# Optimization experiments

Hardware: AMD Instinct MI355X
Metric: run time of the kernel (lower is better)

The kernel has to match this reference:

```python
import jax, jax.numpy as jnp
import numpy as np

B, N, C_IN, C_OUT = 4, 2048, 1024, 1024


def setup_inputs() -> dict:
    key = jax.random.key(0)
    ks = jax.random.split(key, 4)
    scale = 1.0 / np.sqrt(C_IN)
    return {
        "hidden_states": jax.random.normal(ks[0], (B, N, C_IN), dtype=jnp.float32),
        "Wq": jax.random.normal(ks[1], (C_OUT, C_IN), dtype=jnp.float32) * scale,
        "bq": jnp.zeros((C_OUT,), dtype=jnp.float32),
        "Wk": jax.random.normal(ks[2], (C_OUT, C_IN), dtype=jnp.float32) * scale,
        "bk": jnp.zeros((C_OUT,), dtype=jnp.float32),
        "Wv": jax.random.normal(ks[3], (C_OUT, C_IN), dtype=jnp.float32) * scale,
        "bv": jnp.zeros((C_OUT,), dtype=jnp.float32),
    }


def reference(hidden_states, Wq, bq, Wk, bk, Wv, bv):
    # torch nn.Linear: y = x @ W.T + b
    Q = jnp.einsum("bnc,dc->bnd", hidden_states, Wq) + bq
    K = jnp.einsum("bnc,dc->bnd", hidden_states, Wk) + bk
    V = jnp.einsum("bnc,dc->bnd", hidden_states, Wv) + bv
    d_k = K.shape[-1]
    scores = jnp.einsum("bnd,bmd->bnm", Q, K) * (d_k ** -0.5)  # [B,N,N]
    attention = jax.nn.softmax(scores, axis=-1)
    out = jnp.einsum("bnm,bmd->bnd", attention, V)
    return (out, attention)
```

## Files before the change

### kernel.cpp

```cpp
#include <hip/hip_runtime.h>
#include <cstdint>

typedef __attribute__((ext_vector_type(8))) short bf16x8;
typedef __attribute__((ext_vector_type(4))) float f32x4;

__device__ __forceinline__ unsigned short f2bf(float v) {
  unsigned u = __builtin_bit_cast(unsigned, v);
  u += 0x7FFFu + ((u >> 16) & 1u);
  return (unsigned short)(u >> 16);
}

__device__ __forceinline__ void gload16(const unsigned short* g, unsigned short* l) {
  __builtin_amdgcn_global_load_lds(
      (const __attribute__((address_space(1))) void*)(uintptr_t)g,
      (__attribute__((address_space(3))) void*)(uint32_t)(uintptr_t)l,
      16, 0, 0);
}

__device__ __forceinline__ void gemm_core(
    const unsigned short* __restrict__ A, const unsigned short* __restrict__ B,
    int lda, int ldb, int K,
    unsigned short* ldsA, unsigned short* ldsB, f32x4 acc[4][4])
{
  const int tid  = threadIdx.x;
  const int wave = tid >> 6;
  const int lane = tid & 63;
  const int wm = (wave >> 1) * 64;
  const int wn = (wave & 1) * 64;
  const int lrow = lane & 15;
  const int kq = lane >> 4;

  const int sr = lane >> 3;
  const int sc = (lane & 7) ^ (sr & 7);
  const unsigned short* ga = A + (long)(wave * 32 + sr) * lda + sc * 8;
  const unsigned short* gb = B + (long)(wave * 32 + sr) * ldb + sc * 8;
  unsigned short* lA = ldsA + wave * 2048;
  unsigned short* lB = ldsB + wave * 2048;

  const int pc0 = ((0 * 4 + kq) ^ (lrow & 7)) * 8;
  const int pc1 = ((1 * 4 + kq) ^ (lrow & 7)) * 8;

#pragma unroll 1
  for (int kb = 0; kb < K; kb += 64) {
    __syncthreads();
#pragma unroll
    for (int i = 0; i < 4; ++i) {
      gload16(ga + kb + (long)i * 8 * lda, lA + i * 512);
      gload16(gb + kb + (long)i * 8 * ldb, lB + i * 512);
    }
    __syncthreads();

    bf16x8 af[4], bfr[4];
#pragma unroll
    for (int i = 0; i < 4; ++i)
      af[i] = *(const bf16x8*)(ldsA + (wm + i * 16 + lrow) * 64 + pc0);
#pragma unroll
    for (int j = 0; j < 4; ++j)
      bfr[j] = *(const bf16x8*)(ldsB + (wn + j * 16 + lrow) * 64 + pc0);
#pragma unroll
    for (int i = 0; i < 4; ++i)
#pragma unroll
      for (int j = 0; j < 4; ++j)
        acc[i][j] = __builtin_amdgcn_mfma_f32_16x16x32_bf16(af[i], bfr[j], acc[i][j], 0, 0, 0);

#pragma unroll
    for (int i = 0; i < 4; ++i)
      af[i] = *(const bf16x8*)(ldsA + (wm + i * 16 + lrow) * 64 + pc1);
#pragma unroll
    for (int j = 0; j < 4; ++j)
      bfr[j] = *(const bf16x8*)(ldsB + (wn + j * 16 + lrow) * 64 + pc1);
#pragma unroll
    for (int i = 0; i < 4; ++i)
#pragma unroll
      for (int j = 0; j < 4; ++j)
        acc[i][j] = __builtin_amdgcn_mfma_f32_16x16x32_bf16(af[i], bfr[j], acc[i][j], 0, 0, 0);
  }
}

__global__ __launch_bounds__(256, 4) void gemm_qkv(
    const unsigned short* __restrict__ xh,
    const unsigned short* __restrict__ wh,
    const float* __restrict__ bq, const float* __restrict__ bk, const float* __restrict__ bv,
    unsigned short* __restrict__ Qh, unsigned short* __restrict__ Kh,
    unsigned short* __restrict__ Vth)
{
  __shared__ __align__(16) unsigned short ldsA[8192];
  __shared__ __align__(16) unsigned short ldsB[8192];
  const int Mblk = blockIdx.x * 128;
  const int sel  = blockIdx.y >> 3;
  const int nb   = blockIdx.y & 7;

  const unsigned short* A = xh + (long)Mblk * 1024;
  const unsigned short* B = wh + sel * 1048576 + (long)(nb * 128) * 1024;
  const float* bias = (sel == 0) ? bq : (sel == 1) ? bk : bv;

  f32x4 acc[4][4] = {};
  gemm_core(A, B, 1024, 1024, 1024, ldsA, ldsB, acc);

  const int lane = threadIdx.x & 63, wave = threadIdx.x >> 6;
  const int wm = (wave >> 1) * 64, wn = (wave & 1) * 64;
  const int lrow = lane & 15, kq = lane >> 4;

#pragma unroll
  for (int i = 0; i < 4; ++i) {
#pragma unroll
    for (int j = 0; j < 4; ++j) {
      const int col = nb * 128 + wn + j * 16 + lrow;
      const float bsv = bias[col];
#pragma unroll
      for (int r = 0; r < 4; ++r) {
        const int tok = Mblk + wm + i * 16 + kq * 4 + r;
        const unsigned short h = f2bf(acc[i][j][r] + bsv);
        if (sel == 2) {
          Vth[(long)(tok >> 11) * 2097152 + (long)col * 2048 + (tok & 2047)] = h;
        } else if (sel == 0) {
          Qh[(long)tok * 1024 + col] = h;
        } else {
          Kh[(long)tok * 1024 + col] = h;
        }
      }
    }
  }
}

__global__ __launch_bounds__(256, 4) void gemm_f32out(
    const unsigned short* __restrict__ A, const unsigned short* __restrict__ B,
    int lda, int ldb, int K,
    long sA, long sB, float* __restrict__ C, int ldc, long sC, float alpha)
{
  __shared__ __align__(16) unsigned short ldsA[8192];
  __shared__ __align__(16) unsigned short ldsB[8192];
  const int Mblk = blockIdx.x * 128;
  const int Nblk = blockIdx.y * 128;
  const long z = blockIdx.z;
  const unsigned short* Ab = A + z * sA + (long)Mblk * lda;
  const unsigned short* Bb = B + z * sB + (long)Nblk * ldb;
  float* Cb = C + z * sC;

  f32x4 acc[4][4] = {};
  gemm_core(Ab, Bb, lda, ldb, K, ldsA, ldsB, acc);

  const int lane = threadIdx.x & 63, wave = threadIdx.x >> 6;
  const int wm = (wave >> 1) * 64, wn = (wave & 1) * 64;
  const int lrow = lane & 15, kq = lane >> 4;
#pragma unroll
  for (int i = 0; i < 4; ++i)
#pragma unroll
    for (int j = 0; j < 4; ++j)
#pragma unroll
      for (int r = 0; r < 4; ++r) {
        const int row = Mblk + wm + i * 16 + kq * 4 + r;
        const int col = Nblk + wn + j * 16 + lrow;
        Cb[(long)row * ldc + col] = alpha * acc[i][j][r];
      }
}

__global__ __launch_bounds__(256) void softmax_rows(
    float* __restrict__ S, unsigned short* __restrict__ Ph)
{
  __shared__ float red[4];
  const long row = blockIdx.x;
  float* rp = S + row * 2048;
  const int t = threadIdx.x;

  float x[8];
  *(float4*)&x[0] = reinterpret_cast<const float4*>(rp)[t];
  *(float4*)&x[4] = reinterpret_cast<const float4*>(rp)[t + 256];

  float m = x[0];
#pragma unroll
  for (int i = 1; i < 8; ++i) m = fmaxf(m, x[i]);
  for (int o = 32; o; o >>= 1) m = fmaxf(m, __shfl_xor(m, o, 64));
  if ((t & 63) == 0) red[t >> 6] = m;
  __syncthreads();
  m = fmaxf(fmaxf(red[0], red[1]), fmaxf(red[2], red[3]));
  __syncthreads();

  float s = 0.f;
#pragma unroll
  for (int i = 0; i < 8; ++i) { x[i] = expf(x[i] - m); s += x[i]; }
  for (int o = 32; o; o >>= 1) s += __shfl_xor(s, o, 64);
  if ((t & 63) == 0) red[t >> 6] = s;
  __syncthreads();
  s = (red[0] + red[1]) + (red[2] + red[3]);
  const float inv = 1.0f / s;

#pragma unroll
  for (int i = 0; i < 8; ++i) x[i] *= inv;
  reinterpret_cast<float4*>(rp)[t]       = *(float4*)&x[0];
  reinterpret_cast<float4*>(rp)[t + 256] = *(float4*)&x[4];

  const long b0 = row * 2048 + t * 4;
#pragma unroll
  for (int k = 0; k < 4; ++k) Ph[b0 + k] = f2bf(x[k]);
  const long b1 = row * 2048 + 1024 + t * 4;
#pragma unroll
  for (int k = 0; k < 4; ++k) Ph[b1 + k] = f2bf(x[4 + k]);
}

__global__ __launch_bounds__(256) void to_bf16(
    const float* __restrict__ x, unsigned short* __restrict__ hi, int n)
{
  int i = blockIdx.x * 256 + threadIdx.x;
  const int stride = gridDim.x * 256;
  for (; i < n; i += stride) hi[i] = f2bf(x[i]);
}

extern "C" void kernel_launch(void* const* d_in, const int* in_sizes, int n_in,
                              void* d_out, int out_size, void* d_ws, size_t ws_size,
                              hipStream_t stream)
{
  const float* x  = (const float*)d_in[0];
  const float* Wq = (const float*)d_in[1];
  const float* bq = (const float*)d_in[2];
  const float* Wk = (const float*)d_in[3];
  const float* bk = (const float*)d_in[4];
  const float* Wv = (const float*)d_in[5];
  const float* bv = (const float*)d_in[6];

  float* out  = (float*)d_out;
  float* attn = (float*)d_out + 8388608;

  unsigned short* ws  = (unsigned short*)d_ws;
  unsigned short* xh  = ws;
  unsigned short* wh  = xh + 8388608;
  unsigned short* Qh  = wh + 3145728;
  unsigned short* Kh  = Qh + 8388608;
  unsigned short* Vth = Kh + 8388608;
  unsigned short* Ph  = Vth + 8388608;

  to_bf16<<<4096, 256, 0, stream>>>(x, xh, 8388608);
  to_bf16<<<512, 256, 0, stream>>>(Wq, wh, 1048576);
  to_bf16<<<512, 256, 0, stream>>>(Wk, wh + 1048576, 1048576);
  to_bf16<<<512, 256, 0, stream>>>(Wv, wh + 2097152, 1048576);

  gemm_qkv<<<dim3(64, 24), 256, 0, stream>>>(xh, wh, bq, bk, bv, Qh, Kh, Vth);

  gemm_f32out<<<dim3(16, 16, 4), 256, 0, stream>>>(Qh, Kh, 1024, 1024, 1024,
      2097152L, 2097152L, attn, 2048, 4194304L, 0.03125f);

  softmax_rows<<<8192, 256, 0, stream>>>(attn, Ph);

  gemm_f32out<<<dim3(16, 8, 4), 256, 0, stream>>>(Ph, Vth, 2048, 2048, 2048,
      4194304L, 2097152L, out, 1024, 2097152L, 1.0f);
}
```

Before: 317.1 us.

## Double-buffer B tile in LDS and load A fragments directly to registers

Restructures the shared GEMM core so the A operand is loaded straight from global memory into register fragments, with prefetch of the next k-step, instead of being staged through LDS. The B tile is double-buffered in LDS and the next tile is prefetched while MFMAs run on the current one, leaving one barrier per iteration instead of two. This aims to overlap global loads with compute and cut LDS traffic, at the cost of more registers (launch bounds lowered from 4 to 3 waves per SIMD). The direct global loads of A are not coalesced across lanes as well as the LDS path and may duplicate traffic between the waves that share rows.

```diff
diff --git a/kernel.cpp b/kernel.cpp
--- a/kernel.cpp
+++ b/kernel.cpp
@@ -20,7 +20,7 @@
 __device__ __forceinline__ void gemm_core(
     const unsigned short* __restrict__ A, const unsigned short* __restrict__ B,
     int lda, int ldb, int K,
-    unsigned short* ldsA, unsigned short* ldsB, f32x4 acc[4][4])
+    unsigned short* ldsB, f32x4 acc[4][4])
 {
   const int tid  = threadIdx.x;
   const int wave = tid >> 6;
@@ -32,60 +32,75 @@
 
   const int sr = lane >> 3;
   const int sc = (lane & 7) ^ (sr & 7);
-  const unsigned short* ga = A + (long)(wave * 32 + sr) * lda + sc * 8;
   const unsigned short* gb = B + (long)(wave * 32 + sr) * ldb + sc * 8;
-  unsigned short* lA = ldsA + wave * 2048;
   unsigned short* lB = ldsB + wave * 2048;
 
-  const int pc0 = ((0 * 4 + kq) ^ (lrow & 7)) * 8;
-  const int pc1 = ((1 * 4 + kq) ^ (lrow & 7)) * 8;
-
+  const unsigned short* gaBase = A + (long)(wm + lrow) * lda + kq * 8;
+
+  const int pc0 = ((0 + kq) ^ (lrow & 7)) * 8;
+  const int pc1 = ((4 + kq) ^ (lrow & 7)) * 8;
+
+  bf16x8 ar[2][8];
+
+#pragma unroll
+  for (int i = 0; i < 4; ++i)
+    gload16(gb + (long)i * 8 * ldb, lB + i * 512);
+#pragma unroll
+  for (int i = 0; i < 4; ++i) {
+    ar[0][i * 2 + 0] = *(const bf16x8*)(gaBase + (long)(i * 16) * lda);
+    ar[0][i * 2 + 1] = *(const bf16x8*)(gaBase + (long)(i * 16) * lda + 32);
+  }
+  __syncthreads();
+
+  const int nIter = K >> 6;
 #pragma unroll 1
-  for (int kb = 0; kb < K; kb += 64) {
+  for (int it = 0; it < nIter; ++it) {
+    const int cur = it & 1;
+    const unsigned short* bufC = ldsB + cur * 8192;
+
+    if (it + 1 < nIter) {
+      const long kb2 = (long)(it + 1) << 6;
+      unsigned short* bufN = lB + (cur ^ 1) * 8192;
+#pragma unroll
+      for (int i = 0; i < 4; ++i)
+        gload16(gb + kb2 + (long)i * 8 * ldb, bufN + i * 512);
+#pragma unroll
+      for (int i = 0; i < 4; ++i) {
+        ar[cur ^ 1][i * 2 + 0] = *(const bf16x8*)(gaBase + kb2 + (long)(i * 16) * lda);
+        ar[cur ^ 1][i * 2 + 1] = *(const bf16x8*)(gaBase + kb2 + (long)(i * 16) * lda + 32);
+      }
+    }
+
+    bf16x8 bfr[4];
+#pragma unroll
+    for (int j = 0; j < 4; ++j)
+      bfr[j] = *(const bf16x8*)(bufC + (wn + j * 16 + lrow) * 64 + pc0);
+#pragma unroll
+    for (int i = 0; i < 4; ++i)
+#pragma unroll
+      for (int j = 0; j < 4; ++j)
+        acc[i][j] = __builtin_amdgcn_mfma_f32_16x16x32_bf16(ar[cur][i * 2], bfr[j], acc[i][j], 0, 0, 0);
+#pragma unroll
+    for (int j = 0; j < 4; ++j)
+      bfr[j] = *(const bf16x8*)(bufC + (wn + j * 16 + lrow) * 64 + pc1);
+#pragma unroll
+    for (int i = 0; i < 4; ++i)
+#pragma unroll
+      for (int j = 0; j < 4; ++j)
+        acc[i][j] = __builtin_amdgcn_mfma_f32_16x16x32_bf16(ar[cur][i * 2 + 1], bfr[j], acc[i][j], 0, 0, 0);
+
     __syncthreads();
-#pragma unroll
-    for (int i = 0; i < 4; ++i) {
-      gload16(ga + kb + (long)i * 8 * lda, lA + i * 512);
-      gload16(gb + kb + (long)i * 8 * ldb, lB + i * 512);
-    }
-    __syncthreads();
-
-    bf16x8 af[4], bfr[4];
-#pragma unroll
-    for (int i = 0; i < 4; ++i)
-      af[i] = *(const bf16x8*)(ldsA + (wm + i * 16 + lrow) * 64 + pc0);
-#pragma unroll
-    for (int j = 0; j < 4; ++j)
-      bfr[j] = *(const bf16x8*)(ldsB + (wn + j * 16 + lrow) * 64 + pc0);
-#pragma unroll
-    for (int i = 0; i < 4; ++i)
-#pragma unroll
-      for (int j = 0; j < 4; ++j)
-        acc[i][j] = __builtin_amdgcn_mfma_f32_16x16x32_bf16(af[i], bfr[j], acc[i][j], 0, 0, 0);
-
-#pragma unroll
-    for (int i = 0; i < 4; ++i)
-      af[i] = *(const bf16x8*)(ldsA + (wm + i * 16 + lrow) * 64 + pc1);
-#pragma unroll
-    for (int j = 0; j < 4; ++j)
-      bfr[j] = *(const bf16x8*)(ldsB + (wn + j * 16 + lrow) * 64 + pc1);
-#pragma unroll
-    for (int i = 0; i < 4; ++i)
-#pragma unroll
-      for (int j = 0; j < 4; ++j)
-        acc[i][j] = __builtin_amdgcn_mfma_f32_16x16x32_bf16(af[i], bfr[j], acc[i][j], 0, 0, 0);
   }
 }
 
-__global__ __launch_bounds__(256, 4) void gemm_qkv(
+__global__ __launch_bounds__(256, 3) void gemm_qkv(
     const unsigned short* __restrict__ xh,
     const unsigned short* __restrict__ wh,
     const float* __restrict__ bq, const float* __restrict__ bk, const float* __restrict__ bv,
     unsigned short* __restrict__ Qh, unsigned short* __restrict__ Kh,
     unsigned short* __restrict__ Vth)
 {
-  __shared__ __align__(16) unsigned short ldsA[8192];
-  __shared__ __align__(16) unsigned short ldsB[8192];
+  __shared__ __align__(16) unsigned short ldsB[16384];
   const int Mblk = blockIdx.x * 128;
   const int sel  = blockIdx.y >> 3;
   const int nb   = blockIdx.y & 7;
@@ -95,7 +110,7 @@
   const float* bias = (sel == 0) ? bq : (sel == 1) ? bk : bv;
 
   f32x4 acc[4][4] = {};
-  gemm_core(A, B, 1024, 1024, 1024, ldsA, ldsB, acc);
+  gemm_core(A, B, 1024, 1024, 1024, ldsB, acc);
 
   const int lane = threadIdx.x & 63, wave = threadIdx.x >> 6;
   const int wm = (wave >> 1) * 64, wn = (wave & 1) * 64;
@@ -123,13 +138,12 @@
   }
 }
 
-__global__ __launch_bounds__(256, 4) void gemm_f32out(
+__global__ __launch_bounds__(256, 3) void gemm_f32out(
     const unsigned short* __restrict__ A, const unsigned short* __restrict__ B,
     int lda, int ldb, int K,
     long sA, long sB, float* __restrict__ C, int ldc, long sC, float alpha)
 {
-  __shared__ __align__(16) unsigned short ldsA[8192];
-  __shared__ __align__(16) unsigned short ldsB[8192];
+  __shared__ __align__(16) unsigned short ldsB[16384];
   const int Mblk = blockIdx.x * 128;
   const int Nblk = blockIdx.y * 128;
   const long z = blockIdx.z;
@@ -138,7 +152,7 @@
   float* Cb = C + z * sC;
 
   f32x4 acc[4][4] = {};
-  gemm_core(Ab, Bb, lda, ldb, K, ldsA, ldsB, acc);
+  gemm_core(Ab, Bb, lda, ldb, K, ldsB, acc);
 
   const int lane = threadIdx.x & 63, wave = threadIdx.x >> 6;
   const int wm = (wave >> 1) * 64, wn = (wave & 1) * 64;
```

Result: slower. 880.2 us (+177.6%).
